# Kernel tuning notes

Hardware: AMD Instinct MI355X
Metric: run time of the kernel (lower is better)

Reference implementation:

```python
import jax, jax.numpy as jnp
import numpy as np

SCALE = 1.0 / 7.0
EPS = 1e-7


def _pair_iou(b1, b2):
    """Elementwise IoU of cxcywh boxes, faithful to Loss.bboxs_iou (incl. eps placement)."""
    b1x1 = b1[..., 0] - b1[..., 2] * 0.5
    b1x2 = b1[..., 0] + b1[..., 2] * 0.5
    b1y1 = b1[..., 1] - b1[..., 3] * 0.5
    b1y2 = b1[..., 1] + b1[..., 3] * 0.5
    b2x1 = b2[..., 0] - b2[..., 2] * 0.5
    b2x2 = b2[..., 0] + b2[..., 2] * 0.5
    b2y1 = b2[..., 1] - b2[..., 3] * 0.5
    b2y2 = b2[..., 1] + b2[..., 3] * 0.5
    iw = jnp.maximum(jnp.minimum(b1x2, b2x2) - jnp.maximum(b1x1, b2x1), 0.0)
    ih = jnp.maximum(jnp.minimum(b1y2, b2y2) - jnp.maximum(b1y1, b2y1), 0.0)
    inter = iw * ih + EPS
    w1 = b1x2 - b1x1
    h1 = b1y2 - b1y1 + EPS
    w2 = b2x2 - b2x1
    h2 = b2y2 - b2y1 + EPS
    union = w1 * h1 + w2 * h2 - inter + EPS
    return inter / union


def _msum(mask, sq):
    return jnp.sum(jnp.where(mask, sq, 0.0))


def _forward(pre, target):
    B = pre.shape[0]
    pre = pre.reshape(B, 7, 7, 30)
    cell_obj = target[..., 4] > 0       # (B,7,7) grid cells with an object
    cell_noobj = target[..., 4] == 0    # (B,7,7) empty cells

    t_box = target[..., :10].reshape(B, 7, 7, 2, 5)
    p_box = pre[..., :10].reshape(B, 7, 7, 2, 5)

    # per-cell, per-box IoU(pred_b, target_b), b in {0,1}  -> (B,7,7,2)
    iou = _pair_iou(p_box[..., :4], t_box[..., :4])
    resp = jnp.argmax(iou, axis=-1)      # responsible box index (first max, like torch)
    nonresp = jnp.argmin(iou, axis=-1)   # non-responsible box index (first min)

    box_idx = jnp.arange(2)[None, None, None, :]       # (1,1,1,2)
    is_resp = box_idx == resp[..., None]               # (B,7,7,2)
    is_nonresp = box_idx == nonresp[..., None]

    # loop effect 1: zero the confidence of the non-responsible TARGET box
    new_conf = jnp.where(is_nonresp, 0.0, t_box[..., 4])   # (B,7,7,2)

    # loop effect 2: responsible target xy <- normalized offset of the *min-index* box's xy
    xy_nr = jnp.take_along_axis(t_box[..., :2], nonresp[..., None, None], axis=3)  # (B,7,7,1,2)
    xy_nr = xy_nr[..., 0, :]                                                        # (B,7,7,2)
    fxy = (xy_nr - (jnp.ceil(xy_nr / SCALE) - 1.0) * SCALE) / SCALE                 # (B,7,7,2)
    new_xy = jnp.where(is_resp[..., None], fxy[:, :, :, None, :], t_box[..., :2])   # (B,7,7,2,2)

    m_resp = is_resp & cell_obj[..., None]        # responsible boxes of object cells
    m_noresp = (~is_resp) & cell_obj[..., None]   # nomse mask (init 1, cleared at resp)

    loss_xy = _msum(m_resp[..., None], (p_box[..., :2] - new_xy) ** 2)
    loss_wh = _msum(m_resp[..., None],
                    (jnp.sqrt(p_box[..., 2:4] + EPS) - jnp.sqrt(t_box[..., 2:4] + EPS)) ** 2)
    loss_conf = _msum(m_resp, (p_box[..., 4] - new_conf) ** 2)
    loss_noconf = (_msum(m_noresp, (p_box[..., 4] - new_conf) ** 2)
                   + _msum(cell_noobj[..., None], (p_box[..., 4] - t_box[..., 4]) ** 2))
    loss_class = _msum(cell_obj[..., None], (pre[..., 10:] - target[..., 10:]) ** 2)

    loss = 5.0 * (loss_xy + loss_wh) + loss_class + loss_conf + 0.5 * loss_noconf
    return loss / jnp.float32(B)


def setup_inputs() -> dict:
    key = jax.random.key(0)
    k1, k2, k3 = jax.random.split(key, 3)
    B = 16384
    pre = jax.random.uniform(k1, (B, 7 * 7 * 30), dtype=jnp.float32)
    target = jax.random.uniform(k2, (B, 7, 7, 30), dtype=jnp.float32)
    # objectness in {0,1} on both box conf channels so obj/no-obj branches are exercised
    obj = (jax.random.uniform(k3, (B, 7, 7)) > 0.5).astype(jnp.float32)
    target = target.at[..., 4].set(obj).at[..., 9].set(obj)
    return {"pre": pre, "target": target}


def reference(pre, target):
    return _forward(pre, target)
```

## Files before the change

### kernel.cpp

```cpp
#include <hip/hip_runtime.h>

#define EPSF 1e-7f
#define SCALEF (1.0f / 7.0f)

__device__ __forceinline__ float pair_iou(const float* b1, const float* b2) {
    float b1x1 = b1[0] - b1[2] * 0.5f, b1x2 = b1[0] + b1[2] * 0.5f;
    float b1y1 = b1[1] - b1[3] * 0.5f, b1y2 = b1[1] + b1[3] * 0.5f;
    float b2x1 = b2[0] - b2[2] * 0.5f, b2x2 = b2[0] + b2[2] * 0.5f;
    float b2y1 = b2[1] - b2[3] * 0.5f, b2y2 = b2[1] + b2[3] * 0.5f;
    float iw = fmaxf(fminf(b1x2, b2x2) - fmaxf(b1x1, b2x1), 0.0f);
    float ih = fmaxf(fminf(b1y2, b2y2) - fmaxf(b1y1, b2y1), 0.0f);
    float inter = iw * ih + EPSF;
    float w1 = b1x2 - b1x1, h1 = b1y2 - b1y1 + EPSF;
    float w2 = b2x2 - b2x1, h2 = b2y2 - b2y1 + EPSF;
    float uni = w1 * h1 + w2 * h2 - inter + EPSF;
    return inter / uni;
}

__device__ __forceinline__ void gload_lds16(const float4* g, float4* l) {
    __builtin_amdgcn_global_load_lds(
        (const __attribute__((address_space(1))) unsigned int*)g,
        (__attribute__((address_space(3))) unsigned int*)l,
        16, 0, 0);
}

__global__ __launch_bounds__(256) void yolo_loss_partial(
        const float* __restrict__ pre, const float* __restrict__ targ,
        float* __restrict__ partial) {
    __shared__ float4 s4[1920];
    float* sp = reinterpret_cast<float*>(s4);
    float* st = reinterpret_cast<float*>(s4 + 960);
    const int tid = threadIdx.x;
    const int wid = tid >> 6;
    float acc = 0.0f;

#pragma unroll
    for (int chunk = 0; chunk < 2; ++chunk) {
        const size_t base = ((size_t)blockIdx.x * 256 + chunk * 128) * 30;
        const float4* gp = reinterpret_cast<const float4*>(pre + base);
        const float4* gt = reinterpret_cast<const float4*>(targ + base);
        float4* sp4 = s4;
        float4* st4 = s4 + 960;
#pragma unroll
        for (int k = 0; k < 3; ++k) {
            int idx = tid + 256 * k;
            gload_lds16(gp + idx, sp4 + (wid * 64 + 256 * k));
            gload_lds16(gt + idx, st4 + (wid * 64 + 256 * k));
        }
        if (tid < 192) {
            int idx = tid + 768;
            gload_lds16(gp + idx, sp4 + (wid * 64 + 768));
            gload_lds16(gt + idx, st4 + (wid * 64 + 768));
        }
        __syncthreads();

        const int half = tid >> 7;
        const int c = tid & 127;
        const float* cp = sp + c * 30;
        const float* ct = st + c * 30;
        float loss = 0.0f;
        if (half == 0) {
            float p[10], t[10];
            const float2* cp2 = reinterpret_cast<const float2*>(cp);
            const float2* ct2 = reinterpret_cast<const float2*>(ct);
#pragma unroll
            for (int i = 0; i < 5; ++i) {
                float2 a = cp2[i]; p[2 * i] = a.x; p[2 * i + 1] = a.y;
                float2 b = ct2[i]; t[2 * i] = b.x; t[2 * i + 1] = b.y;
            }
            bool cell_obj   = t[4] > 0.0f;
            bool cell_noobj = t[4] == 0.0f;
            float iou0 = pair_iou(p + 0, t + 0);
            float iou1 = pair_iou(p + 5, t + 5);
            int resp    = (iou1 > iou0) ? 1 : 0;
            int nonresp = (iou1 < iou0) ? 1 : 0;
            float xnr = nonresp ? t[5] : t[0];
            float ynr = nonresp ? t[6] : t[1];
            float fx = (xnr - (ceilf(xnr / SCALEF) - 1.0f) * SCALEF) / SCALEF;
            float fy = (ynr - (ceilf(ynr / SCALEF) - 1.0f) * SCALEF) / SCALEF;
            float lxy = 0.0f, lwh = 0.0f, lconf = 0.0f, lnoconf = 0.0f;
#pragma unroll
            for (int i = 0; i < 2; ++i) {
                const float* pb = p + i * 5;
                const float* tb = t + i * 5;
                bool is_resp    = (i == resp);
                bool is_nonresp = (i == nonresp);
                float new_conf = is_nonresp ? 0.0f : tb[4];
                if (cell_obj) {
                    if (is_resp) {
                        float dx = pb[0] - fx, dy = pb[1] - fy;
                        lxy += dx * dx + dy * dy;
                        float dw = sqrtf(pb[2] + EPSF) - sqrtf(tb[2] + EPSF);
                        float dh = sqrtf(pb[3] + EPSF) - sqrtf(tb[3] + EPSF);
                        lwh += dw * dw + dh * dh;
                        float dc = pb[4] - new_conf;
                        lconf += dc * dc;
                    } else {
                        float dc = pb[4] - new_conf;
                        lnoconf += dc * dc;
                    }
                }
                if (cell_noobj) {
                    float dc = pb[4] - tb[4];
                    lnoconf += dc * dc;
                }
            }
            loss = 5.0f * (lxy + lwh) + lconf + 0.5f * lnoconf;
        } else {
            float tobj = ct[4];
            if (tobj > 0.0f) {
                float s = 0.0f;
                const float2* cp2 = reinterpret_cast<const float2*>(cp + 10);
                const float2* ct2 = reinterpret_cast<const float2*>(ct + 10);
#pragma unroll
                for (int i = 0; i < 10; ++i) {
                    float2 a = cp2[i], b = ct2[i];
                    float d0 = a.x - b.x, d1 = a.y - b.y;
                    s += d0 * d0 + d1 * d1;
                }
                loss = s;
            }
        }
        acc += loss;
        __syncthreads();
    }

#pragma unroll
    for (int off = 32; off > 0; off >>= 1) acc += __shfl_down(acc, off, 64);
    __shared__ float ssum[4];
    int lane = tid & 63;
    if (lane == 0) ssum[wid] = acc;
    __syncthreads();
    if (tid == 0) partial[blockIdx.x] = ssum[0] + ssum[1] + ssum[2] + ssum[3];
}

__global__ __launch_bounds__(256) void yolo_loss_final(
        const float* __restrict__ partial, int n, float invB, float* __restrict__ out) {
    float v = 0.0f;
    for (int i = threadIdx.x; i < n; i += 256) v += partial[i];
#pragma unroll
    for (int off = 32; off > 0; off >>= 1) v += __shfl_down(v, off, 64);
    __shared__ float ssum[4];
    int lane = threadIdx.x & 63, wid = threadIdx.x >> 6;
    if (lane == 0) ssum[wid] = v;
    __syncthreads();
    if (threadIdx.x == 0) out[0] = (ssum[0] + ssum[1] + ssum[2] + ssum[3]) * invB;
}

extern "C" void kernel_launch(void* const* d_in, const int* in_sizes, int n_in,
                              void* d_out, int out_size, void* d_ws, size_t ws_size,
                              hipStream_t stream) {
    const float* pre  = (const float*)d_in[0];
    const float* targ = (const float*)d_in[1];
    float* out = (float*)d_out;
    float* partial = (float*)d_ws;

    int B = in_sizes[0] / 1470;
    int n_cells = B * 49;
    int nblocks = n_cells / 256;

    yolo_loss_partial<<<nblocks, 256, 0, stream>>>(pre, targ, partial);
    yolo_loss_final<<<1, 256, 0, stream>>>(partial, nblocks, 1.0f / (float)B, out);
}
```

Measured before the change: 38.08 us.

## Double-buffer LDS staging across eight 64-cell chunks per block

Each block now covers 512 cells in eight 64-cell chunks. Chunks are staged through two LDS buffers, so the global-to-LDS loads for the next chunk are in flight while the current chunk is computed. Explicit vmcnt waits and raw s_barrier replace the full __syncthreads. Work is split so wave 0 does the box terms, waves 1–2 each do half the class terms, and wave 3 only loads. The launch uses half as many blocks, which lowers parallelism across CUs in exchange for overlapping memory and compute within each block.

```diff
diff --git a/kernel.cpp b/kernel.cpp
--- a/kernel.cpp
+++ b/kernel.cpp
@@ -24,42 +24,46 @@
         16, 0, 0);
 }
 
+__device__ __forceinline__ void stage_chunk(const float4* gp, const float4* gt,
+                                            float4* buf, int tid, int wid) {
+    gload_lds16(gp + tid,       buf + wid * 64);
+    if (tid < 224)
+        gload_lds16(gp + 256 + tid, buf + 256 + wid * 64);
+    gload_lds16(gt + tid,       buf + 480 + wid * 64);
+    if (tid < 224)
+        gload_lds16(gt + 256 + tid, buf + 480 + 256 + wid * 64);
+}
+
 __global__ __launch_bounds__(256) void yolo_loss_partial(
         const float* __restrict__ pre, const float* __restrict__ targ,
         float* __restrict__ partial) {
-    __shared__ float4 s4[1920];
-    float* sp = reinterpret_cast<float*>(s4);
-    float* st = reinterpret_cast<float*>(s4 + 960);
+    __shared__ float4 s4[2][960];
     const int tid = threadIdx.x;
     const int wid = tid >> 6;
+    const int lane = tid & 63;
+
+    const size_t cell0 = (size_t)blockIdx.x * 512;
+    const float4* gp = reinterpret_cast<const float4*>(pre  + cell0 * 30);
+    const float4* gt = reinterpret_cast<const float4*>(targ + cell0 * 30);
     float acc = 0.0f;
 
+    stage_chunk(gp, gt, &s4[0][0], tid, wid);
+
 #pragma unroll
-    for (int chunk = 0; chunk < 2; ++chunk) {
-        const size_t base = ((size_t)blockIdx.x * 256 + chunk * 128) * 30;
-        const float4* gp = reinterpret_cast<const float4*>(pre + base);
-        const float4* gt = reinterpret_cast<const float4*>(targ + base);
-        float4* sp4 = s4;
-        float4* st4 = s4 + 960;
-#pragma unroll
-        for (int k = 0; k < 3; ++k) {
-            int idx = tid + 256 * k;
-            gload_lds16(gp + idx, sp4 + (wid * 64 + 256 * k));
-            gload_lds16(gt + idx, st4 + (wid * 64 + 256 * k));
-        }
-        if (tid < 192) {
-            int idx = tid + 768;
-            gload_lds16(gp + idx, sp4 + (wid * 64 + 768));
-            gload_lds16(gt + idx, st4 + (wid * 64 + 768));
-        }
-        __syncthreads();
+    for (int c = 0; c < 8; ++c) {
+        if (c < 7)
+            stage_chunk(gp + (size_t)(c + 1) * 480, gt + (size_t)(c + 1) * 480,
+                        &s4[(c + 1) & 1][0], tid, wid);
+        if (c < 7) { asm volatile("s_waitcnt vmcnt(4)" ::: "memory"); }
+        else       { asm volatile("s_waitcnt vmcnt(0)" ::: "memory"); }
+        __builtin_amdgcn_s_barrier();
+        __builtin_amdgcn_sched_barrier(0);
 
-        const int half = tid >> 7;
-        const int c = tid & 127;
-        const float* cp = sp + c * 30;
-        const float* ct = st + c * 30;
+        const float* bufF = reinterpret_cast<const float*>(&s4[c & 1][0]);
         float loss = 0.0f;
-        if (half == 0) {
+        if (wid == 0) {
+            const float* cp = bufF + lane * 30;
+            const float* ct = bufF + 1920 + lane * 30;
             float p[10], t[10];
             const float2* cp2 = reinterpret_cast<const float2*>(cp);
             const float2* ct2 = reinterpret_cast<const float2*>(ct);
@@ -106,14 +110,16 @@
                 }
             }
             loss = 5.0f * (lxy + lwh) + lconf + 0.5f * lnoconf;
-        } else {
-            float tobj = ct[4];
-            if (tobj > 0.0f) {
+        } else if (wid < 3) {
+            int q = tid - 64;
+            int cc = q & 63, h = q >> 6;
+            const float* ct = bufF + 1920 + cc * 30;
+            if (ct[4] > 0.0f) {
+                const float2* cp2 = reinterpret_cast<const float2*>(bufF + cc * 30 + 10 + h * 10);
+                const float2* ct2 = reinterpret_cast<const float2*>(ct + 10 + h * 10);
                 float s = 0.0f;
-                const float2* cp2 = reinterpret_cast<const float2*>(cp + 10);
-                const float2* ct2 = reinterpret_cast<const float2*>(ct + 10);
 #pragma unroll
-                for (int i = 0; i < 10; ++i) {
+                for (int i = 0; i < 5; ++i) {
                     float2 a = cp2[i], b = ct2[i];
                     float d0 = a.x - b.x, d1 = a.y - b.y;
                     s += d0 * d0 + d1 * d1;
@@ -122,13 +128,12 @@
             }
         }
         acc += loss;
-        __syncthreads();
+        if (c < 7) __builtin_amdgcn_s_barrier();
     }
 
 #pragma unroll
     for (int off = 32; off > 0; off >>= 1) acc += __shfl_down(acc, off, 64);
     __shared__ float ssum[4];
-    int lane = tid & 63;
     if (lane == 0) ssum[wid] = acc;
     __syncthreads();
     if (tid == 0) partial[blockIdx.x] = ssum[0] + ssum[1] + ssum[2] + ssum[3];
@@ -157,7 +162,7 @@
 
     int B = in_sizes[0] / 1470;
     int n_cells = B * 49;
-    int nblocks = n_cells / 256;
+    int nblocks = n_cells / 512;
 
     yolo_loss_partial<<<nblocks, 256, 0, stream>>>(pre, targ, partial);
     yolo_loss_final<<<1, 256, 0, stream>>>(partial, nblocks, 1.0f / (float)B, out);
```

After: 39.54 us. 1.04x slower.
